# Kernel optimization log

Hardware: AMD Instinct MI355X
Metric: run time of the kernel (lower is better)

## Reference

```python
import jax, jax.numpy as jnp
import numpy as np
from jax import lax

# LNS semantics: values are held as (sign, log_base|x|); exact conversion round-trips
# make log-domain mul/add mathematically identical to float conv/linear/relu, so the
# faithful reference is the equivalent float pipeline.

def _conv(x, w, b):
    # x: [B,C,H,W], w: [O,C,kh,kw] (torch layout), stride 1, no padding
    y = lax.conv_general_dilated(x, w, window_strides=(1, 1), padding='VALID',
                                 dimension_numbers=('NCHW', 'OIHW', 'NCHW'))
    return y + b[None, :, None, None]

def _maxpool2(x):
    return lax.reduce_window(x, -jnp.inf, lax.max,
                             window_dimensions=(1, 1, 2, 2),
                             window_strides=(1, 1, 2, 2), padding='VALID')

def setup_inputs() -> dict:
    key = jax.random.key(0)
    ks = jax.random.split(key, 9)
    s = lambda k, shape, fan: jax.random.normal(k, shape, jnp.float32) * (1.0 / np.sqrt(fan))
    return {
        'x': jax.random.normal(ks[0], (512, 1, 54, 54), jnp.float32),
        'conv1_w': s(ks[1], (32, 1, 3, 3), 9),
        'conv1_b': s(ks[2], (32,), 9),
        'conv2_w': s(ks[3], (64, 32, 3, 3), 32 * 9),
        'conv2_b': s(ks[4], (64,), 32 * 9),
        'fc1_w': s(ks[5], (128, 9216), 9216),
        'fc1_b': s(ks[6], (128,), 9216),
        'fc2_w': s(ks[7], (10, 128), 128),
        'fc2_b': s(ks[8], (10,), 128),
    }

def reference(x, conv1_w, conv1_b, conv2_w, conv2_b, fc1_w, fc1_b, fc2_w, fc2_b):
    h = jnp.maximum(_conv(x, conv1_w, conv1_b), 0.0)          # [B,32,52,52]
    h = _maxpool2(h)                                          # [B,32,26,26]
    h = jnp.maximum(_conv(h, conv2_w, conv2_b), 0.0)          # [B,64,24,24]
    h = _maxpool2(h)                                          # [B,64,12,12]
    h = h.reshape(h.shape[0], -1)                             # [B,9216]
    h = jnp.maximum(h @ fc1_w.T + fc1_b, 0.0)                 # [B,128]
    return h @ fc2_w.T + fc2_b                                # [B,10]
```

## Files before the change

kernel.cpp:

```cpp
#include <hip/hip_runtime.h>


#define B 512
#define POS 676
#define ICP 36
#define P2SZ (64*12*12)
#define SCR 26

typedef unsigned short ushort_t;
typedef ushort_t ushort4v __attribute__((ext_vector_type(4)));
typedef short s16x8 __attribute__((ext_vector_type(8)));
typedef float f32x4 __attribute__((ext_vector_type(4)));
typedef float f32x2 __attribute__((ext_vector_type(2)));

__device__ __forceinline__ ushort_t f2bf(float f) {
    union { float f; unsigned u; } a; a.f = f;
    unsigned r = a.u + 0x7FFFu + ((a.u >> 16) & 1u);
    return (ushort_t)(r >> 16);
}
__device__ __forceinline__ float bf2f(ushort_t u) {
    union { unsigned u; float f; } a; a.u = ((unsigned)u) << 16;
    return a.f;
}

#define N_WR (64 * 9 * 32)
#define CONV1_BLOCKS 3328
#define WR_BLOCKS 72
#define TR_BLOCKS 128

__global__ __launch_bounds__(256) void conv1_prep(const float* __restrict__ x,
                                                  const float* __restrict__ w,
                                                  const float* __restrict__ bias,
                                                  const float* __restrict__ c2w,
                                                  const float* __restrict__ f1w,
                                                  ushort_t* __restrict__ out,
                                                  ushort_t* __restrict__ wr,
                                                  ushort_t* __restrict__ wfb) {
    __shared__ float tr[64 * 145];
    int blk = blockIdx.x;
    int tid = threadIdx.x;

    if (blk >= CONV1_BLOCKS + WR_BLOCKS) {
        int n = blk - CONV1_BLOCKS - WR_BLOCKS;
        const float* src = f1w + (size_t)n * 9216;
#pragma unroll
        for (int i = 0; i < 36; ++i) {
            int idx = i * 256 + tid;
            int oc = idx / 144, pos = idx - oc * 144;
            tr[oc * 145 + pos] = src[idx];
        }
        __syncthreads();
        ushort_t* dst = wfb + (size_t)n * 9216;
#pragma unroll
        for (int i = 0; i < 36; ++i) {
            int idx = i * 256 + tid;
            int pos = idx >> 6, oc = idx & 63;
            dst[idx] = f2bf(tr[oc * 145 + pos]);
        }
        return;
    }
    if (blk >= CONV1_BLOCKS) {
        int t = (blk - CONV1_BLOCKS) * 256 + tid;
        int ic  = t & 31;
        int tap = (t >> 5) % 9;
        int oc  = t / 288;
        wr[t] = f2bf(c2w[oc * 288 + ic * 9 + tap]);
        return;
    }
    int t = blk * 256 + tid;
    int ic = t & 31;
    int r  = t >> 5;
    int h  = r & 1;
    int r2 = r >> 1;
    int py = r2 % 26;
    int b  = r2 / 26;
    int px0 = h * 13;

    const float* wp = w + ic * 9;
    float w00 = wp[0], w01 = wp[1], w02 = wp[2];
    float w10 = wp[3], w11 = wp[4], w12 = wp[5];
    float w20 = wp[6], w21 = wp[7], w22 = wp[8];
    float bv = bias[ic];

    const float* xr = x + b * (54 * 54) + (2 * py) * 54 + 2 * px0;
    ushort_t* po = out + ((size_t)b * POS + py * 26 + px0) * 32 + ic;

    f32x2 p[4], q[4];
#pragma unroll
    for (int rr = 0; rr < 4; ++rr) p[rr] = *reinterpret_cast<const f32x2*>(xr + rr * 54);
#pragma unroll
    for (int rr = 0; rr < 4; ++rr) q[rr] = *reinterpret_cast<const f32x2*>(xr + rr * 54 + 2);

#pragma unroll
    for (int j = 0; j < 13; ++j) {
        f32x2 mid[4];
#pragma unroll
        for (int rr = 0; rr < 4; ++rr) mid[rr] = (f32x2){p[rr].y, q[rr].x};

        f32x2 s0 = p[0] * (f32x2)w00 + mid[0] * (f32x2)w01 + q[0] * (f32x2)w02
                 + p[1] * (f32x2)w10 + mid[1] * (f32x2)w11 + q[1] * (f32x2)w12
                 + p[2] * (f32x2)w20 + mid[2] * (f32x2)w21 + q[2] * (f32x2)w22;
        f32x2 s1 = p[1] * (f32x2)w00 + mid[1] * (f32x2)w01 + q[1] * (f32x2)w02
                 + p[2] * (f32x2)w10 + mid[2] * (f32x2)w11 + q[2] * (f32x2)w12
                 + p[3] * (f32x2)w20 + mid[3] * (f32x2)w21 + q[3] * (f32x2)w22;

        float m = fmaxf(fmaxf(s0.x, s0.y), fmaxf(s1.x, s1.y));
        po[j * 32] = f2bf(fmaxf(m + bv, 0.0f));
        if (j < 12) {
#pragma unroll
            for (int rr = 0; rr < 4; ++rr) {
                p[rr] = q[rr];
                q[rr] = *reinterpret_cast<const f32x2*>(xr + rr * 54 + 2 * j + 4);
            }
        }
    }
}

__global__ __launch_bounds__(512) void conv2_mfma(const ushort_t* __restrict__ p1,
                                                  const ushort_t* __restrict__ wr,
                                                  const float* __restrict__ bias,
                                                  ushort_t* __restrict__ pool2cl) {
    __shared__ ushort_t lds[260 * ICP];
    int blk = blockIdx.x;
    int b = blk / 3, c = blk % 3;
    int tid = threadIdx.x;

    const ushort_t* src = p1 + ((size_t)b * POS + 8 * c * 26) * 32;
    for (int t = tid; t < 260 * 8; t += 512) {
        int pos = t >> 3, off = (t & 7) * 4;
        ushort4v v = *reinterpret_cast<const ushort4v*>(src + pos * 32 + off);
        *reinterpret_cast<ushort4v*>(&lds[pos * ICP + off]) = v;
    }
    __syncthreads();

    int lane = tid & 63, wid = tid >> 6;
    int quad = lane >> 4, lr = lane & 15;
    int prow = wid >> 1;
    int nhalf = wid & 1;

    int ebase[3];
#pragma unroll
    for (int t = 0; t < 3; ++t) {
        int m  = t * 16 + lr;
        int yl = m / 24;
        int xx = m - yl * 24;
        ebase[t] = ((2 * prow + yl) * 26 + xx) * ICP + quad * 8;
    }

    f32x4 acc[3][2];
#pragma unroll
    for (int t = 0; t < 3; ++t)
#pragma unroll
        for (int n = 0; n < 2; ++n) acc[t][n] = (f32x4){0.f, 0.f, 0.f, 0.f};

    const ushort_t* wb = wr + (size_t)(nhalf * 32 + lr) * 288 + quad * 8;

#pragma unroll
    for (int tap = 0; tap < 9; ++tap) {
        int ky = tap / 3, kx = tap % 3;
        int koff = (ky * 26 + kx) * ICP;
        s16x8 a[3];
#pragma unroll
        for (int t = 0; t < 3; ++t) {
            union { ushort4v s[2]; s16x8 v; } u;
            u.s[0] = *reinterpret_cast<const ushort4v*>(&lds[ebase[t] + koff]);
            u.s[1] = *reinterpret_cast<const ushort4v*>(&lds[ebase[t] + koff + 4]);
            a[t] = u.v;
        }
        s16x8 bf[2];
#pragma unroll
        for (int n = 0; n < 2; ++n)
            bf[n] = *reinterpret_cast<const s16x8*>(wb + (size_t)n * 16 * 288 + tap * 32);
#pragma unroll
        for (int t = 0; t < 3; ++t)
#pragma unroll
            for (int n = 0; n < 2; ++n)
                acc[t][n] = __builtin_amdgcn_mfma_f32_16x16x32_bf16(a[t], bf[n], acc[t][n], 0, 0, 0);
    }
    __syncthreads();

    ushort_t* scr = lds + wid * (32 * SCR);
#pragma unroll
    for (int t = 0; t < 3; ++t)
#pragma unroll
        for (int n = 0; n < 2; ++n) {
            int ocl = n * 16 + lr;
            int i0 = t * 8 + quad * 2;
            float v0 = fmaxf(acc[t][n][0], acc[t][n][1]);
            float v1 = fmaxf(acc[t][n][2], acc[t][n][3]);
            union { ushort_t u2[2]; unsigned w; } pk;
            pk.u2[0] = f2bf(v0); pk.u2[1] = f2bf(v1);
            *reinterpret_cast<unsigned*>(&scr[ocl * SCR + i0]) = pk.w;
        }
    int ocl = lane & 31;
    int pxh = lane >> 5;
    int oc  = nhalf * 32 + ocl;
    const ushort_t* row = scr + ocl * SCR;
    float bv = bias[oc];
    int py = c * 4 + prow;
    ushort_t* po = pool2cl + ((size_t)b * 144 + py * 12) * 64 + oc;
#pragma unroll
    for (int j = 0; j < 6; ++j) {
        int px = pxh * 6 + j;
        float r0 = bf2f(row[px]);
        float r1 = bf2f(row[px + 12]);
        po[px * 64] = f2bf(fmaxf(fmaxf(r0, r1) + bv, 0.0f));
    }
}

__global__ __launch_bounds__(256) void fc1_mfma(const ushort_t* __restrict__ A,
                                                 const ushort_t* __restrict__ W,
                                                 float* __restrict__ Cpart) {
    int tid = threadIdx.x;
    int lane = tid & 63, wid = tid >> 6;
    int lr = lane & 15, quad = lane >> 4;
    int w  = blockIdx.x * 4 + wid;
    int nt = w & 3;
    int ks = (w >> 2) & 15;
    int mt = w >> 6;

    int m0 = mt * 16;
    int n0 = nt * 32;
    int k0 = ks * 576 + quad * 8;
    const ushort_t* a0 = A + (size_t)(m0 + lr) * 9216 + k0;
    const ushort_t* b0 = W + (size_t)(n0 + lr) * 9216 + k0;
    const ushort_t* b1 = b0 + (size_t)16 * 9216;

    f32x4 acc0 = (f32x4){0.f, 0.f, 0.f, 0.f};
    f32x4 acc1 = (f32x4){0.f, 0.f, 0.f, 0.f};

#pragma unroll
    for (int kk = 0; kk < 18; ++kk) {
        s16x8 av  = *reinterpret_cast<const s16x8*>(a0 + kk * 32);
        s16x8 bv0 = *reinterpret_cast<const s16x8*>(b0 + kk * 32);
        s16x8 bv1 = *reinterpret_cast<const s16x8*>(b1 + kk * 32);
        acc0 = __builtin_amdgcn_mfma_f32_16x16x32_bf16(av, bv0, acc0, 0, 0, 0);
        acc1 = __builtin_amdgcn_mfma_f32_16x16x32_bf16(av, bv1, acc1, 0, 0, 0);
    }

    float* cp = Cpart + (size_t)ks * (512 * 128);
    int crow = m0 + quad * 4;
#pragma unroll
    for (int r = 0; r < 4; ++r) {
        cp[(size_t)(crow + r) * 128 + n0 + lr]      = acc0[r];
        cp[(size_t)(crow + r) * 128 + n0 + 16 + lr] = acc1[r];
    }
}

__global__ __launch_bounds__(256) void fc1fc2(const float* __restrict__ Cpart,
                                              const float* __restrict__ b1,
                                              const float* __restrict__ w2,
                                              const float* __restrict__ b2,
                                              float* __restrict__ out) {
    __shared__ float h[2][128];
    int half = threadIdx.x >> 7;
    int k = threadIdx.x & 127;
    int b = blockIdx.x * 2 + half;
    float s = 0.f;
#pragma unroll
    for (int ks = 0; ks < 16; ++ks) s += Cpart[(size_t)ks * (512 * 128) + b * 128 + k];
    h[half][k] = fmaxf(s + b1[k], 0.0f);
    __syncthreads();
    if (k < 10) {
        const float* wp = w2 + k * 128;
        float acc = 0.f;
#pragma unroll 8
        for (int j = 0; j < 128; ++j) acc += h[half][j] * wp[j];
        out[b * 10 + k] = acc + b2[k];
    }
}

extern "C" void kernel_launch(void* const* d_in, const int* in_sizes, int n_in,
                              void* d_out, int out_size, void* d_ws, size_t ws_size,
                              hipStream_t stream) {
    const float* x       = (const float*)d_in[0];
    const float* conv1_w = (const float*)d_in[1];
    const float* conv1_b = (const float*)d_in[2];
    const float* conv2_w = (const float*)d_in[3];
    const float* conv2_b = (const float*)d_in[4];
    const float* fc1_w   = (const float*)d_in[5];
    const float* fc1_b   = (const float*)d_in[6];
    const float* fc2_w   = (const float*)d_in[7];
    const float* fc2_b   = (const float*)d_in[8];
    float* out = (float*)d_out;

    char* ws = (char*)d_ws;
    ushort_t* pool1 = (ushort_t*)ws;
    ws += (size_t)B * POS * 32 * sizeof(ushort_t);
    ushort_t* wr = (ushort_t*)ws;
    ws += N_WR * sizeof(ushort_t) + 128;
    ushort_t* wfb = (ushort_t*)ws;
    ws += (size_t)128 * 9216 * sizeof(ushort_t) + 128;
    ushort_t* pool2cl = (ushort_t*)ws;
    ws += (size_t)B * P2SZ * sizeof(ushort_t) + 128;
    float* Cpart = (float*)ws;
    ws += (size_t)16 * 512 * 128 * sizeof(float) + 128;

    conv1_prep<<<CONV1_BLOCKS + WR_BLOCKS + TR_BLOCKS, 256, 0, stream>>>(
        x, conv1_w, conv1_b, conv2_w, fc1_w, pool1, wr, wfb);
    conv2_mfma<<<B * 3, 512, 0, stream>>>(pool1, wr, conv2_b, pool2cl);
    fc1_mfma<<<512, 256, 0, stream>>>(pool2cl, wfb, Cpart);
    fc1fc2<<<256, 256, 0, stream>>>(Cpart, fc1_b, fc2_w, fc2_b, out);
}
```

Before: 131.8 us.

## Rewrite conv1 as bf16 MFMA over an LDS-staged image

The conv1+relu+pool stage moves from per-thread scalar FMA stencils reading global memory to a block-per-half-image scheme. Each block stages the bf16-converted image in LDS, with a shifted copy so odd columns can be read with aligned dword loads, and computes the 3x3 taps with 16x16x32 bf16 MFMA instructions. Each 3-tap row is padded to 8 K slots, so most of the MFMA work multiplies zeros. The input is now rounded to bf16 before the convolution, which adds precision loss. Block count drops from 3328 to 1024, which changes occupancy and load balance for this stage.

```diff
diff --git a/kernel.cpp b/kernel.cpp
--- a/kernel.cpp
+++ b/kernel.cpp
@@ -6,12 +6,13 @@
 #define ICP 36
 #define P2SZ (64*12*12)
 #define SCR 26
+#define IMS 58
+#define IMCOPY (54 * IMS)
 
 typedef unsigned short ushort_t;
 typedef ushort_t ushort4v __attribute__((ext_vector_type(4)));
 typedef short s16x8 __attribute__((ext_vector_type(8)));
 typedef float f32x4 __attribute__((ext_vector_type(4)));
-typedef float f32x2 __attribute__((ext_vector_type(2)));
 
 __device__ __forceinline__ ushort_t f2bf(float f) {
     union { float f; unsigned u; } a; a.f = f;
@@ -24,7 +25,7 @@
 }
 
 #define N_WR (64 * 9 * 32)
-#define CONV1_BLOCKS 3328
+#define CONV1_BLOCKS 1024
 #define WR_BLOCKS 72
 #define TR_BLOCKS 128
 
@@ -36,11 +37,12 @@
                                                   ushort_t* __restrict__ out,
                                                   ushort_t* __restrict__ wr,
                                                   ushort_t* __restrict__ wfb) {
-    __shared__ float tr[64 * 145];
+    __shared__ char smem[64 * 145 * 4];
     int blk = blockIdx.x;
     int tid = threadIdx.x;
 
     if (blk >= CONV1_BLOCKS + WR_BLOCKS) {
+        float* tr = reinterpret_cast<float*>(smem);
         int n = blk - CONV1_BLOCKS - WR_BLOCKS;
         const float* src = f1w + (size_t)n * 9216;
 #pragma unroll
@@ -67,50 +69,75 @@
         wr[t] = f2bf(c2w[oc * 288 + ic * 9 + tap]);
         return;
     }
-    int t = blk * 256 + tid;
-    int ic = t & 31;
-    int r  = t >> 5;
-    int h  = r & 1;
-    int r2 = r >> 1;
-    int py = r2 % 26;
-    int b  = r2 / 26;
-    int px0 = h * 13;
-
-    const float* wp = w + ic * 9;
-    float w00 = wp[0], w01 = wp[1], w02 = wp[2];
-    float w10 = wp[3], w11 = wp[4], w12 = wp[5];
-    float w20 = wp[6], w21 = wp[7], w22 = wp[8];
-    float bv = bias[ic];
-
-    const float* xr = x + b * (54 * 54) + (2 * py) * 54 + 2 * px0;
-    ushort_t* po = out + ((size_t)b * POS + py * 26 + px0) * 32 + ic;
-
-    f32x2 p[4], q[4];
-#pragma unroll
-    for (int rr = 0; rr < 4; ++rr) p[rr] = *reinterpret_cast<const f32x2*>(xr + rr * 54);
-#pragma unroll
-    for (int rr = 0; rr < 4; ++rr) q[rr] = *reinterpret_cast<const f32x2*>(xr + rr * 54 + 2);
-
-#pragma unroll
-    for (int j = 0; j < 13; ++j) {
-        f32x2 mid[4];
-#pragma unroll
-        for (int rr = 0; rr < 4; ++rr) mid[rr] = (f32x2){p[rr].y, q[rr].x};
-
-        f32x2 s0 = p[0] * (f32x2)w00 + mid[0] * (f32x2)w01 + q[0] * (f32x2)w02
-                 + p[1] * (f32x2)w10 + mid[1] * (f32x2)w11 + q[1] * (f32x2)w12
-                 + p[2] * (f32x2)w20 + mid[2] * (f32x2)w21 + q[2] * (f32x2)w22;
-        f32x2 s1 = p[1] * (f32x2)w00 + mid[1] * (f32x2)w01 + q[1] * (f32x2)w02
-                 + p[2] * (f32x2)w10 + mid[2] * (f32x2)w11 + q[2] * (f32x2)w12
-                 + p[3] * (f32x2)w20 + mid[3] * (f32x2)w21 + q[3] * (f32x2)w22;
-
-        float m = fmaxf(fmaxf(s0.x, s0.y), fmaxf(s1.x, s1.y));
-        po[j * 32] = f2bf(fmaxf(m + bv, 0.0f));
-        if (j < 12) {
-#pragma unroll
-            for (int rr = 0; rr < 4; ++rr) {
-                p[rr] = q[rr];
-                q[rr] = *reinterpret_cast<const f32x2*>(xr + rr * 54 + 2 * j + 4);
+
+    ushort_t* lds = reinterpret_cast<ushort_t*>(smem);
+    int b    = blk >> 1;
+    int half = blk & 1;
+
+    const float* xim = x + (size_t)b * 2916;
+    for (int i = tid; i < 2916; i += 256) {
+        int r = i / 54, c = i - r * 54;
+        ushort_t v = f2bf(xim[i]);
+        lds[r * IMS + c] = v;
+        if (c > 0) lds[IMCOPY + r * IMS + c - 1] = v;
+    }
+
+    int lane = tid & 63, wid = tid >> 6;
+    int quad = lane >> 4, lr = lane & 15;
+
+    s16x8 bfrag[2];
+#pragma unroll
+    for (int n = 0; n < 2; ++n) {
+        union { ushort_t u[8]; s16x8 v; } bu;
+#pragma unroll
+        for (int j = 0; j < 8; ++j) bu.u[j] = 0;
+        if (quad < 3) {
+            const float* wp = w + (n * 16 + lr) * 9 + quad * 3;
+            bu.u[0] = f2bf(wp[0]);
+            bu.u[1] = f2bf(wp[1]);
+            bu.u[2] = f2bf(wp[2]);
+        }
+        bfrag[n] = bu.v;
+    }
+    float bv0 = bias[lr], bv1 = bias[16 + lr];
+
+    __syncthreads();
+
+    int cbase = (lr & 1) ? (IMCOPY + lr - 1) : lr;
+
+    for (int py_l = wid; py_l < 13; py_l += 4) {
+        int py = half * 13 + py_l;
+        int y0 = 2 * py;
+#pragma unroll
+        for (int t = 0; t < 4; ++t) {
+            int x0 = t * 16;
+            int off0 = cbase + x0 + (y0 + quad) * IMS;
+            int off1 = off0 + IMS;
+            union { unsigned d[4]; s16x8 v; } a0, a1;
+            a0.d[0] = *reinterpret_cast<const unsigned*>(&lds[off0]);
+            a0.d[1] = *reinterpret_cast<const unsigned*>(&lds[off0 + 2]);
+            a0.d[2] = a0.d[0]; a0.d[3] = a0.d[1];
+            a1.d[0] = *reinterpret_cast<const unsigned*>(&lds[off1]);
+            a1.d[1] = *reinterpret_cast<const unsigned*>(&lds[off1 + 2]);
+            a1.d[2] = a1.d[0]; a1.d[3] = a1.d[1];
+
+            f32x4 cA0 = (f32x4){0.f,0.f,0.f,0.f}, cA1 = cA0, cB0 = cA0, cB1 = cA0;
+            cA0 = __builtin_amdgcn_mfma_f32_16x16x32_bf16(a0.v, bfrag[0], cA0, 0, 0, 0);
+            cA1 = __builtin_amdgcn_mfma_f32_16x16x32_bf16(a0.v, bfrag[1], cA1, 0, 0, 0);
+            cB0 = __builtin_amdgcn_mfma_f32_16x16x32_bf16(a1.v, bfrag[0], cB0, 0, 0, 0);
+            cB1 = __builtin_amdgcn_mfma_f32_16x16x32_bf16(a1.v, bfrag[1], cB1, 0, 0, 0);
+
+            if (t < 3 || quad == 0) {
+                int px0 = t * 8 + quad * 2;
+                float u0 = fmaxf(fmaxf(cA0[0], cA0[1]), fmaxf(cB0[0], cB0[1]));
+                float u1 = fmaxf(fmaxf(cA0[2], cA0[3]), fmaxf(cB0[2], cB0[3]));
+                float v0 = fmaxf(fmaxf(cA1[0], cA1[1]), fmaxf(cB1[0], cB1[1]));
+                float v1 = fmaxf(fmaxf(cA1[2], cA1[3]), fmaxf(cB1[2], cB1[3]));
+                ushort_t* po = out + ((size_t)b * POS + py * 26 + px0) * 32;
+                po[lr]           = f2bf(fmaxf(u0 + bv0, 0.0f));
+                po[32 + lr]      = f2bf(fmaxf(u1 + bv0, 0.0f));
+                po[16 + lr]      = f2bf(fmaxf(v0 + bv1, 0.0f));
+                po[32 + 16 + lr] = f2bf(fmaxf(v1 + bv1, 0.0f));
             }
         }
     }
```

Result: faster. 127.7 us (median of 2 runs) (-3.1%).
